# Optimization experiments

Measured on AMD Instinct MI355X. Metric: run time of the kernel, lower is better.

Reference implementation:

```python
import jax, jax.numpy as jnp
import numpy as np
from jax import lax


def _conv2d(x, w, b):
    # 3x3 conv, stride 1, pad 1, NCHW / OIHW
    out = lax.conv_general_dilated(x, w, (1, 1), ((1, 1), (1, 1)),
                                   dimension_numbers=('NCHW', 'OIHW', 'NCHW'))
    return out + b[None, :, None, None]


def _bilinear(img, py, px):
    # img: [C,H,W]; py,px: [K2,Ho,Wo] float sample coords -> [C,K2,Ho,Wo]
    H, W = img.shape[-2], img.shape[-1]
    y0 = jnp.floor(py); x0 = jnp.floor(px)
    wy1 = py - y0; wy0 = 1.0 - wy1
    wx1 = px - x0; wx0 = 1.0 - wx1

    def corner(yi, xi):
        valid = (yi >= 0) & (yi <= H - 1) & (xi >= 0) & (xi <= W - 1)
        yc = jnp.clip(yi, 0, H - 1).astype(jnp.int32)
        xc = jnp.clip(xi, 0, W - 1).astype(jnp.int32)
        return img[:, yc, xc] * valid.astype(img.dtype)  # [C,K2,Ho,Wo]

    return (wy0 * wx0 * corner(y0, x0) + wy0 * wx1 * corner(y0, x0 + 1)
            + wy1 * wx0 * corner(y0 + 1, x0) + wy1 * wx1 * corner(y0 + 1, x0 + 1))


def setup_inputs() -> dict:
    key = jax.random.key(0)
    ks = jax.random.split(key, 7)
    B, C, H, W = 8, 64, 128, 128
    O, K = 64, 3
    x = jax.random.normal(ks[0], (B, C, H, W), jnp.float32)
    # offset branch (torch init was zeros; use small random so offsets are nontrivial)
    w_off = jax.random.normal(ks[1], (2 * K * K, C, 3, 3), jnp.float32) * 0.01
    b_off = jax.random.normal(ks[2], (2 * K * K,), jnp.float32) * 0.01
    w_mask = jax.random.normal(ks[3], (K * K, C, 3, 3), jnp.float32) * 0.05
    b_mask = jnp.zeros((K * K,), jnp.float32)
    w_dcn = jax.random.normal(ks[4], (O, C, K, K), jnp.float32) * (1.0 / np.sqrt(C * K * K))
    b_dcn = jax.random.normal(ks[5], (O,), jnp.float32) * 0.01
    return {'x': x, 'w_off': w_off, 'b_off': b_off, 'w_mask': w_mask,
            'b_mask': b_mask, 'w_dcn': w_dcn, 'b_dcn': b_dcn}


def reference(x, w_off, b_off, w_mask, b_mask, w_dcn, b_dcn):
    B, C, H, W = x.shape
    K = 3; K2 = K * K; pad = 1; stride = 1
    offset = _conv2d(x, w_off, b_off)                 # [B,2*K2,H,W]
    mask = jax.nn.sigmoid(_conv2d(x, w_mask, b_mask))  # [B,K2,H,W]
    off = offset.reshape(B, K2, 2, H, W)
    dy, dx = off[:, :, 0], off[:, :, 1]               # [B,K2,H,W]
    ki = (jnp.arange(K2) // K).astype(x.dtype)
    kj = (jnp.arange(K2) % K).astype(x.dtype)
    base_y = jnp.arange(H, dtype=x.dtype)[None, :, None] * stride - pad + ki[:, None, None]  # [K2,H,1]
    base_x = jnp.arange(W, dtype=x.dtype)[None, None, :] * stride - pad + kj[:, None, None]  # [K2,1,W]
    py = base_y + dy                                   # [B,K2,H,W]
    px = base_x + dx
    sampled = jax.vmap(_bilinear)(x, py, px)           # [B,C,K2,H,W]
    sampled = sampled * mask[:, None]
    O = w_dcn.shape[0]
    out = jnp.einsum('bckhw,ock->bohw', sampled, w_dcn.reshape(O, C, K2))
    return out + b_dcn[None, :, None, None]
```

## Files before the change

kernel.cpp:

```cpp
#include <hip/hip_runtime.h>
#include <hip/hip_bf16.h>
#include <math.h>

#define Bt 8
#define Ct 64
#define Ht 128
#define Wt 128
#define Ot 64
#define HWt (Ht*Wt)

#define BROWS 20
#define BCOLS 12
#define BPX   240
#define WBUF_U 15360
#define ODM_B  38912
#define ODM_S  27

typedef __bf16 bf16x8 __attribute__((ext_vector_type(8)));
typedef float  f32x4  __attribute__((ext_vector_type(4)));

__device__ __forceinline__ uint f2bf_bits(float v) {
    uint u = __float_as_uint(v);
    uint lsb = (u >> 16) & 1u;
    return (u + 0x7fffu + lsb) >> 16;
}
__device__ __forceinline__ ushort f2bf(float v) {
    return (ushort)f2bf_bits(v);
}

__device__ __forceinline__ uint4 band_read(const ushort* smem, uint pIdx, uint chunkB) {
    uint off = pIdx * 128u + (chunkB ^ ((pIdx & 7u) << 4));
    return *(const uint4*)((const char*)smem + off);
}

__global__ __launch_bounds__(256) void prep_kernel(
    const float* __restrict__ x, const float* __restrict__ w_off,
    const float* __restrict__ w_mask, const float* __restrict__ w_dcn,
    ushort* __restrict__ xTb, ushort* __restrict__ wOffB, ushort* __restrict__ wMainB)
{
    int blk = blockIdx.x;
    int t = threadIdx.x;
    if (blk < 1024) {
        __shared__ float L[64][128];
        int b = blk & 7, y = blk >> 3;
        const float* xb = x + (size_t)b * 1048576 + y * 128;
#pragma unroll
        for (int it = 0; it < 8; ++it) {
            int i = it * 256 + t;
            int c = i >> 5, x4 = i & 31;
            *(float4*)&L[c][x4 * 4] = *(const float4*)&xb[(size_t)c * HWt + x4 * 4];
        }
        __syncthreads();
        int px = t >> 1, half = (t & 1) * 32;
        union { ushort u[32]; uint4 q[4]; } pk;
#pragma unroll
        for (int i = 0; i < 32; ++i) pk.u[i] = f2bf(L[half + i][px]);
        uint4* dst = (uint4*)(xTb + ((size_t)(b * 128 + y) * 128 + px) * 64 + half);
        dst[0] = pk.q[0]; dst[1] = pk.q[1]; dst[2] = pk.q[2]; dst[3] = pk.q[3];
    } else {
        int i = (blk - 1024) * 256 + t;
        if (i < 9 * 32 * 64) {
            int c = i & 63, ch = (i >> 6) & 31, k = i >> 11;
            float v = 0.f;
            if (ch < 18)      v = w_off[(ch * 64 + c) * 9 + k];
            else if (ch < 27) v = w_mask[((ch - 18) * 64 + c) * 9 + k];
            wOffB[i] = f2bf(v);
        } else {
            int j = i - 18432;
            if (j < 9 * 64 * 64) {
                int c = j & 63, o = (j >> 6) & 63, k = j >> 12;
                wMainB[j] = f2bf(w_dcn[(o * 64 + c) * 9 + k]);
            }
        }
    }
}

struct Tap { float w[4]; int pix[4]; uint gof[4]; uint inb; };

__device__ __forceinline__ void tap_ctx(int k, int ry, float cxf, int cq8,
                                        int row0, int col0,
                                        const float* __restrict__ odmRow, Tap& tp) {
    int ky = k / 3, kx = k - ky * 3;
    float dyv = odmRow[k];
    float dxv = odmRow[9 + k];
    float mkv = odmRow[18 + k];
    float py  = (float)(ry + ky - 1) + dyv;
    float pxf = cxf + (float)(kx - 1) + dxv;
    float y0f = floorf(py), x0f = floorf(pxf);
    float wy1 = py - y0f, wy0 = 1.f - wy1;
    float wx1 = pxf - x0f, wx0 = 1.f - wx1;
    bool vy0 = (y0f >= 0.f) && (y0f <= 127.f);
    bool vy1 = (y0f >= -1.f) && (y0f <= 126.f);
    bool vx0 = (x0f >= 0.f) && (x0f <= 127.f);
    bool vx1 = (x0f >= -1.f) && (x0f <= 126.f);
    tp.w[0] = (vy0 && vx0) ? wy0 * wx0 * mkv : 0.f;
    tp.w[1] = (vy0 && vx1) ? wy0 * wx1 * mkv : 0.f;
    tp.w[2] = (vy1 && vx0) ? wy1 * wx0 * mkv : 0.f;
    tp.w[3] = (vy1 && vx1) ? wy1 * wx1 * mkv : 0.f;
    int yi0 = (int)y0f, xi0 = (int)x0f;
    int y0c = min(max(yi0, 0), 127), y1c = min(max(yi0 + 1, 0), 127);
    int x0c = min(max(xi0, 0), 127), x1c = min(max(xi0 + 1, 0), 127);
    int by0 = y0c - row0, by1 = y1c - row0;
    int bx0 = x0c - col0, bx1 = x1c - col0;
    bool ry0 = (unsigned)by0 < (unsigned)BROWS, ry1 = (unsigned)by1 < (unsigned)BROWS;
    bool rx0 = (unsigned)bx0 < (unsigned)BCOLS, rx1 = (unsigned)bx1 < (unsigned)BCOLS;
    tp.inb = (uint)(ry0 && rx0) | ((uint)(ry0 && rx1) << 1)
           | ((uint)(ry1 && rx0) << 2) | ((uint)(ry1 && rx1) << 3);
    tp.pix[0] = by0 * BCOLS + bx0;
    tp.pix[1] = by0 * BCOLS + bx1;
    tp.pix[2] = by1 * BCOLS + bx0;
    tp.pix[3] = by1 * BCOLS + bx1;
    tp.gof[0] = (uint)(((y0c << 7) + x0c) * 64 + cq8);
    tp.gof[1] = (uint)(((y0c << 7) + x1c) * 64 + cq8);
    tp.gof[2] = (uint)(((y1c << 7) + x0c) * 64 + cq8);
    tp.gof[3] = (uint)(((y1c << 7) + x1c) * 64 + cq8);
}

__device__ __forceinline__ void tap_blend(const Tap& tp, const uint4* D, bf16x8* afr) {
    float w00 = tp.w[0], w01 = tp.w[1], w10 = tp.w[2], w11 = tp.w[3];
#pragma unroll
    for (int ks = 0; ks < 2; ++ks) {
        union { uint4 q; uint u[4]; } v00, v01, v10, v11, wr;
        v00.q = D[0 * 2 + ks];
        v01.q = D[1 * 2 + ks];
        v10.q = D[2 * 2 + ks];
        v11.q = D[3 * 2 + ks];
#pragma unroll
        for (int j = 0; j < 4; ++j) {
            float f00l = __uint_as_float(v00.u[j] << 16);
            float f00h = __uint_as_float(v00.u[j] & 0xffff0000u);
            float f01l = __uint_as_float(v01.u[j] << 16);
            float f01h = __uint_as_float(v01.u[j] & 0xffff0000u);
            float f10l = __uint_as_float(v10.u[j] << 16);
            float f10h = __uint_as_float(v10.u[j] & 0xffff0000u);
            float f11l = __uint_as_float(v11.u[j] << 16);
            float f11h = __uint_as_float(v11.u[j] & 0xffff0000u);
            float vl = w00 * f00l;
            vl = fmaf(w01, f01l, vl); vl = fmaf(w10, f10l, vl); vl = fmaf(w11, f11l, vl);
            float vh = w00 * f00h;
            vh = fmaf(w01, f01h, vh); vh = fmaf(w10, f10h, vh); vh = fmaf(w11, f11h, vh);
            wr.u[j] = (f2bf_bits(vh) << 16) | f2bf_bits(vl);
        }
        afr[ks] = __builtin_bit_cast(bf16x8, wr.q);
    }
}

__global__ __launch_bounds__(512, 6) void dcn_fused_kernel(
    const ushort* __restrict__ xTb, const ushort* __restrict__ wOffB,
    const ushort* __restrict__ wMainB, const float* __restrict__ b_off,
    const float* __restrict__ b_mask, const float* __restrict__ b_dcn,
    float* __restrict__ out)
{
    __shared__ ushort smem[26368];
    float* odmF = (float*)((char*)smem + ODM_B);

    int t = threadIdx.x;
    int blk = blockIdx.x;
    int b = blk & 7;
    int tile = blk >> 3;
    int rowBase = (tile >> 4) * 16;
    int colBase = (tile & 15) * 8;
    int wv = t >> 6, ln = t & 63;
    int m = ln & 15, cq = ln >> 4;
    int cq8 = cq * 8;
    int prow = 2 * wv + (m >> 3);
    int pcol = m & 7;
    int ry = rowBase + prow;
    int cx = colBase + pcol;

    const ushort* xbb = xTb + (size_t)b * 1048576;

#pragma unroll
    for (int it = 0; it < 4; ++it) {
        int j = it * 512 + t;
        if (j < BPX * 8) {
            int pIdx = j >> 3, ch8 = j & 7;
            int br = pIdx / BCOLS, bc = pIdx - br * BCOLS;
            int iy = min(max(rowBase - 2 + br, 0), 127);
            int ix = min(max(colBase - 2 + bc, 0), 127);
            *(uint4*)((char*)smem + pIdx * 128 + ((ch8 * 16) ^ ((pIdx & 7) << 4))) =
                *(const uint4*)&xbb[(size_t)((iy << 7) + ix) * 64 + ch8 * 8];
        }
    }
    {
        int r = t >> 3, gch = t & 7;
        *(uint4*)&smem[WBUF_U + r * 64 + ((gch + r) & 7) * 8] =
            *(const uint4*)&wOffB[(size_t)r * 64 + gch * 8];
    }
    __syncthreads();

    f32x4 acc0 = {0.f, 0.f, 0.f, 0.f};
    f32x4 acc1 = {0.f, 0.f, 0.f, 0.f};
#pragma unroll
    for (int kp = 0; kp < 5; ++kp) {
        if (kp > 0) {
            __syncthreads();
            const int nchunks = (kp == 4) ? 256 : 512;
            if (t < nchunks) {
                int r = t >> 3, gch = t & 7;
                *(uint4*)&smem[WBUF_U + r * 64 + ((gch + r) & 7) * 8] =
                    *(const uint4*)&wOffB[(size_t)(kp * 64 + r) * 64 + gch * 8];
            }
            __syncthreads();
        }
#pragma unroll
        for (int tl = 0; tl < 2; ++tl) {
            const int k = kp * 2 + tl;
            if (k <= 8) {
                int ky = k / 3, kx = k - ky * 3;
                int iyr = prow + ky - 1;
                int ixr = pcol + kx - 1;
                bool ok = ((unsigned)(rowBase + iyr) < 128u) && ((unsigned)(colBase + ixr) < 128u);
                uint pIdx = (uint)((iyr + 2) * BCOLS + (ixr + 2));
                uint4 a0 = band_read(smem, pIdx, cq8 * 2);
                uint4 a1 = band_read(smem, pIdx, cq8 * 2 + 64);
                if (!ok) { a0 = uint4{0u,0u,0u,0u}; a1 = uint4{0u,0u,0u,0u}; }
                int lbr0 = tl * 32 + m;
                int lbr1 = lbr0 + 16;
#pragma unroll
                for (int ks = 0; ks < 2; ++ks) {
                    bf16x8 afr = __builtin_bit_cast(bf16x8, ks ? a1 : a0);
                    int gs = ks * 4 + cq;
                    bf16x8 b0 = __builtin_bit_cast(bf16x8,
                        *(const uint4*)&smem[WBUF_U + lbr0 * 64 + ((gs + lbr0) & 7) * 8]);
                    bf16x8 b1 = __builtin_bit_cast(bf16x8,
                        *(const uint4*)&smem[WBUF_U + lbr1 * 64 + ((gs + lbr1) & 7) * 8]);
                    acc0 = __builtin_amdgcn_mfma_f32_16x16x32_bf16(afr, b0, acc0, 0, 0, 0);
                    acc1 = __builtin_amdgcn_mfma_f32_16x16x32_bf16(afr, b1, acc1, 0, 0, 0);
                }
            }
        }
    }

    {
        int n = m;
        int pxl = wv * 16 + (cq << 2);
#pragma unroll
        for (int r = 0; r < 4; ++r) {
            int pp = pxl + r;
            odmF[pp * ODM_S + (n & 1) * 9 + (n >> 1)] = acc0[r] + b_off[n];
            int ch = 16 + n;
            float v1 = acc1[r];
            if (ch < 18) {
                odmF[pp * ODM_S + (ch & 1) * 9 + (ch >> 1)] = v1 + b_off[ch];
            } else if (ch < 27) {
                float val = v1 + b_mask[ch - 18];
                odmF[pp * ODM_S + 18 + (ch - 18)] = 1.f / (1.f + __expf(-val));
            }
        }
    }
    __syncthreads();

    {
        int r = t >> 3, gch = t & 7;
        *(uint4*)&smem[WBUF_U + r * 64 + ((gch + r) & 7) * 8] =
            *(const uint4*)&wMainB[(size_t)r * 64 + gch * 8];
    }
    __syncthreads();

    f32x4 acc[4];
#pragma unroll
    for (int i = 0; i < 4; ++i) acc[i] = f32x4{0.f, 0.f, 0.f, 0.f};

    float cxf = (float)cx;
    const float* odmRow = odmF + (wv * 16 + m) * ODM_S;
    const int row0 = rowBase - 2, col0 = colBase - 2;

#pragma unroll
    for (int k = 0; k < 9; ++k) {
        if (k > 0) {
            __syncthreads();
            int r = t >> 3, gch = t & 7;
            *(uint4*)&smem[WBUF_U + r * 64 + ((gch + r) & 7) * 8] =
                *(const uint4*)&wMainB[(size_t)(k * 64 + r) * 64 + gch * 8];
            __syncthreads();
        }

        Tap tp;
        tap_ctx(k, ry, cxf, cq8, row0, col0, odmRow, tp);

        uint4 D[8];
#pragma unroll
        for (int c = 0; c < 4; ++c) {
            bool ib = (tp.inb >> c) & 1u;
            uint pS = ib ? (uint)tp.pix[c] : 0u;
            D[c * 2]     = band_read(smem, pS, cq8 * 2);
            D[c * 2 + 1] = band_read(smem, pS, cq8 * 2 + 64);
            if (!ib) {
                D[c * 2]     = *(const uint4*)(xbb + tp.gof[c]);
                D[c * 2 + 1] = *(const uint4*)(xbb + tp.gof[c] + 32);
            }
        }

        bf16x8 afr[2];
        tap_blend(tp, D, afr);

#pragma unroll
        for (int ks = 0; ks < 2; ++ks) {
            int chk = ks * 4 + cq;
#pragma unroll
            for (int nt = 0; nt < 4; ++nt) {
                int lrow = nt * 16 + m;
                bf16x8 bb = __builtin_bit_cast(bf16x8,
                    *(const uint4*)&smem[WBUF_U + lrow * 64 + ((chk + lrow) & 7) * 8]);
                acc[nt] = __builtin_amdgcn_mfma_f32_16x16x32_bf16(afr[ks], bb, acc[nt], 0, 0, 0);
            }
        }
    }

#pragma unroll
    for (int nt = 0; nt < 4; ++nt) {
        int o = nt * 16 + m;
        float bias = b_dcn[o];
        float4 v;
        v.x = acc[nt][0] + bias;
        v.y = acc[nt][1] + bias;
        v.z = acc[nt][2] + bias;
        v.w = acc[nt][3] + bias;
        float* orow = out + ((size_t)(b * 64 + o) << 14)
                    + (rowBase + 2 * wv + (cq >> 1)) * 128 + colBase + (cq & 1) * 4;
        *(float4*)orow = v;
    }
}

extern "C" void kernel_launch(void* const* d_in, const int* in_sizes, int n_in,
                              void* d_out, int out_size, void* d_ws, size_t ws_size,
                              hipStream_t stream) {
    const float* x      = (const float*)d_in[0];
    const float* w_off  = (const float*)d_in[1];
    const float* b_off  = (const float*)d_in[2];
    const float* w_mask = (const float*)d_in[3];
    const float* b_mask = (const float*)d_in[4];
    const float* w_dcn  = (const float*)d_in[5];
    const float* b_dcn  = (const float*)d_in[6];
    float* out = (float*)d_out;

    ushort* xTb    = (ushort*)d_ws;
    ushort* wOffB  = xTb + (size_t)Bt * HWt * 64;
    ushort* wMainB = wOffB + 18432;

    hipLaunchKernelGGL(prep_kernel, dim3(1024 + 216), dim3(256), 0, stream,
                       x, w_off, w_mask, w_dcn, xTb, wOffB, wMainB);
    hipLaunchKernelGGL(dcn_fused_kernel, dim3(1024), dim3(512), 0, stream,
                       xTb, wOffB, wMainB, b_off, b_mask, b_dcn, out);
}
```

Before: 146.4 us.

## Drop bf16 NHWC transpose pass and read fp32 NCHW input directly in fused kernel

```diff
diff --git a/kernel.cpp b/kernel.cpp
--- a/kernel.cpp
+++ b/kernel.cpp
@@ -34,50 +34,29 @@
 }
 
 __global__ __launch_bounds__(256) void prep_kernel(
-    const float* __restrict__ x, const float* __restrict__ w_off,
-    const float* __restrict__ w_mask, const float* __restrict__ w_dcn,
-    ushort* __restrict__ xTb, ushort* __restrict__ wOffB, ushort* __restrict__ wMainB)
+    const float* __restrict__ w_off, const float* __restrict__ w_mask,
+    const float* __restrict__ w_dcn,
+    ushort* __restrict__ wOffB, ushort* __restrict__ wMainB)
 {
-    int blk = blockIdx.x;
-    int t = threadIdx.x;
-    if (blk < 1024) {
-        __shared__ float L[64][128];
-        int b = blk & 7, y = blk >> 3;
-        const float* xb = x + (size_t)b * 1048576 + y * 128;
-#pragma unroll
-        for (int it = 0; it < 8; ++it) {
-            int i = it * 256 + t;
-            int c = i >> 5, x4 = i & 31;
-            *(float4*)&L[c][x4 * 4] = *(const float4*)&xb[(size_t)c * HWt + x4 * 4];
-        }
-        __syncthreads();
-        int px = t >> 1, half = (t & 1) * 32;
-        union { ushort u[32]; uint4 q[4]; } pk;
-#pragma unroll
-        for (int i = 0; i < 32; ++i) pk.u[i] = f2bf(L[half + i][px]);
-        uint4* dst = (uint4*)(xTb + ((size_t)(b * 128 + y) * 128 + px) * 64 + half);
-        dst[0] = pk.q[0]; dst[1] = pk.q[1]; dst[2] = pk.q[2]; dst[3] = pk.q[3];
+    int i = blockIdx.x * 256 + threadIdx.x;
+    if (i < 9 * 32 * 64) {
+        int c = i & 63, ch = (i >> 6) & 31, k = i >> 11;
+        float v = 0.f;
+        if (ch < 18)      v = w_off[(ch * 64 + c) * 9 + k];
+        else if (ch < 27) v = w_mask[((ch - 18) * 64 + c) * 9 + k];
+        wOffB[i] = f2bf(v);
     } else {
-        int i = (blk - 1024) * 256 + t;
-        if (i < 9 * 32 * 64) {
-            int c = i & 63, ch = (i >> 6) & 31, k = i >> 11;
-            float v = 0.f;
-            if (ch < 18)      v = w_off[(ch * 64 + c) * 9 + k];
-            else if (ch < 27) v = w_mask[((ch - 18) * 64 + c) * 9 + k];
-            wOffB[i] = f2bf(v);
-        } else {
-            int j = i - 18432;
-            if (j < 9 * 64 * 64) {
-                int c = j & 63, o = (j >> 6) & 63, k = j >> 12;
-                wMainB[j] = f2bf(w_dcn[(o * 64 + c) * 9 + k]);
-            }
-        }
-    }
-}
-
-struct Tap { float w[4]; int pix[4]; uint gof[4]; uint inb; };
-
-__device__ __forceinline__ void tap_ctx(int k, int ry, float cxf, int cq8,
+        int j = i - 18432;
+        if (j < 9 * 64 * 64) {
+            int c = j & 63, o = (j >> 6) & 63, k = j >> 12;
+            wMainB[j] = f2bf(w_dcn[(o * 64 + c) * 9 + k]);
+        }
+    }
+}
+
+struct Tap { float w[4]; int pix[4]; int pixg[4]; uint inb; };
+
+__device__ __forceinline__ void tap_ctx(int k, int ry, float cxf,
                                         int row0, int col0,
                                         const float* __restrict__ odmRow, Tap& tp) {
     int ky = k / 3, kx = k - ky * 3;
@@ -110,10 +89,10 @@
     tp.pix[1] = by0 * BCOLS + bx1;
     tp.pix[2] = by1 * BCOLS + bx0;
     tp.pix[3] = by1 * BCOLS + bx1;
-    tp.gof[0] = (uint)(((y0c << 7) + x0c) * 64 + cq8);
-    tp.gof[1] = (uint)(((y0c << 7) + x1c) * 64 + cq8);
-    tp.gof[2] = (uint)(((y1c << 7) + x0c) * 64 + cq8);
-    tp.gof[3] = (uint)(((y1c << 7) + x1c) * 64 + cq8);
+    tp.pixg[0] = (y0c << 7) + x0c;
+    tp.pixg[1] = (y0c << 7) + x1c;
+    tp.pixg[2] = (y1c << 7) + x0c;
+    tp.pixg[3] = (y1c << 7) + x1c;
 }
 
 __device__ __forceinline__ void tap_blend(const Tap& tp, const uint4* D, bf16x8* afr) {
@@ -146,7 +125,7 @@
 }
 
 __global__ __launch_bounds__(512, 6) void dcn_fused_kernel(
-    const ushort* __restrict__ xTb, const ushort* __restrict__ wOffB,
+    const float* __restrict__ x, const ushort* __restrict__ wOffB,
     const ushort* __restrict__ wMainB, const float* __restrict__ b_off,
     const float* __restrict__ b_mask, const float* __restrict__ b_dcn,
     float* __restrict__ out)
@@ -168,18 +147,22 @@
     int ry = rowBase + prow;
     int cx = colBase + pcol;
 
-    const ushort* xbb = xTb + (size_t)b * 1048576;
+    const float* xbf = x + (size_t)b * 1048576;
 
 #pragma unroll
     for (int it = 0; it < 4; ++it) {
         int j = it * 512 + t;
         if (j < BPX * 8) {
-            int pIdx = j >> 3, ch8 = j & 7;
+            int ch8 = j / 240;
+            int pIdx = j - ch8 * 240;
             int br = pIdx / BCOLS, bc = pIdx - br * BCOLS;
             int iy = min(max(rowBase - 2 + br, 0), 127);
             int ix = min(max(colBase - 2 + bc, 0), 127);
-            *(uint4*)((char*)smem + pIdx * 128 + ((ch8 * 16) ^ ((pIdx & 7) << 4))) =
-                *(const uint4*)&xbb[(size_t)((iy << 7) + ix) * 64 + ch8 * 8];
+            const float* xs = xbf + (size_t)(ch8 * 8) * HWt + (iy << 7) + ix;
+            union { ushort us[8]; uint4 q; } pk;
+#pragma unroll
+            for (int u = 0; u < 8; ++u) pk.us[u] = f2bf(xs[(size_t)u * HWt]);
+            *(uint4*)((char*)smem + pIdx * 128 + ((ch8 * 16) ^ ((pIdx & 7) << 4))) = pk.q;
         }
     }
     {
@@ -277,7 +260,7 @@
         }
 
         Tap tp;
-        tap_ctx(k, ry, cxf, cq8, row0, col0, odmRow, tp);
+        tap_ctx(k, ry, cxf, row0, col0, odmRow, tp);
 
         uint4 D[8];
 #pragma unroll
@@ -287,8 +270,14 @@
             D[c * 2]     = band_read(smem, pS, cq8 * 2);
             D[c * 2 + 1] = band_read(smem, pS, cq8 * 2 + 64);
             if (!ib) {
-                D[c * 2]     = *(const uint4*)(xbb + tp.gof[c]);
-                D[c * 2 + 1] = *(const uint4*)(xbb + tp.gof[c] + 32);
+#pragma unroll
+                for (int ks = 0; ks < 2; ++ks) {
+                    const float* xc = xbf + (size_t)(cq8 + ks * 32) * HWt + tp.pixg[c];
+                    union { ushort us[8]; uint4 q; } pk;
+#pragma unroll
+                    for (int u = 0; u < 8; ++u) pk.us[u] = f2bf(xc[(size_t)u * HWt]);
+                    D[c * 2 + ks] = pk.q;
+                }
             }
         }
 
@@ -335,12 +324,11 @@
     const float* b_dcn  = (const float*)d_in[6];
     float* out = (float*)d_out;
 
-    ushort* xTb    = (ushort*)d_ws;
-    ushort* wOffB  = xTb + (size_t)Bt * HWt * 64;
+    ushort* wOffB  = (ushort*)d_ws;
     ushort* wMainB = wOffB + 18432;
 
-    hipLaunchKernelGGL(prep_kernel, dim3(1024 + 216), dim3(256), 0, stream,
-                       x, w_off, w_mask, w_dcn, xTb, wOffB, wMainB);
+    hipLaunchKernelGGL(prep_kernel, dim3(216), dim3(256), 0, stream,
+                       w_off, w_mask, w_dcn, wOffB, wMainB);
     hipLaunchKernelGGL(dcn_fused_kernel, dim3(1024), dim3(512), 0, stream,
-                       xTb, wOffB, wMainB, b_off, b_mask, b_dcn, out);
-}
+                       x, wOffB, wMainB, b_off, b_mask, b_dcn, out);
+}
```

Result: faster. 141.9 us (-3.0%).
